# Kernel tuning notes

Hardware: AMD Instinct MI355X
Metric: run time of the kernel (lower is better)

The kernel has to match this reference:

```python
import jax, jax.numpy as jnp
import numpy as np
from jax import lax

B, C, H, W = 4, 128, 128, 128
DG = 2          # deformable groups
K = 9           # 3x3 kernel
EPS = 1e-5


def conv2d(x, w, stride=1, pad=1):
    return lax.conv_general_dilated(
        x, w, (stride, stride), [(pad, pad), (pad, pad)],
        dimension_numbers=("NCHW", "OIHW", "NCHW"))


def bn(x, p):
    # p: [4, C] = gamma, beta, running_mean, running_var (eval-mode BN)
    g, b, m, v = p[0], p[1], p[2], p[3]
    inv = g / jnp.sqrt(v + EPS)
    return x * inv[:, None, None] + (b - m * inv)[:, None, None]


def deform_sample(x, py, px):
    # x: [B,C,H,W]; py/px: [B,DG,K,H,W] absolute sample coords
    Bb, Cc, Hh, Ww = x.shape
    Cg = Cc // DG
    xg = x.reshape(Bb, DG, Cg, Hh * Ww)
    y0 = jnp.floor(py); x0 = jnp.floor(px)
    fy = py - y0; fx = px - x0
    y0i = y0.astype(jnp.int32); x0i = x0.astype(jnp.int32)

    def corner(yi, xi, wgt):
        valid = (yi >= 0) & (yi < Hh) & (xi >= 0) & (xi < Ww)
        idx = (jnp.clip(yi, 0, Hh - 1) * Ww + jnp.clip(xi, 0, Ww - 1)).reshape(Bb, DG, -1)
        v = jnp.take_along_axis(xg, idx[:, :, None, :], axis=3)  # [B,DG,Cg,K*H*W]
        return v * (wgt * valid).reshape(Bb, DG, 1, -1)

    val = (corner(y0i, x0i, (1 - fy) * (1 - fx))
           + corner(y0i, x0i + 1, (1 - fy) * fx)
           + corner(y0i + 1, x0i, fy * (1 - fx))
           + corner(y0i + 1, x0i + 1, fy * fx))
    return val.reshape(Bb, DG, Cg, K, Hh, Ww)


def modulated_deform_conv(x, off_w, off_b, dc_w, dc_b):
    Bb, Cc, Hh, Ww = x.shape
    off_out = conv2d(x, off_w) + off_b[None, :, None, None]   # [B,3*DG*K,H,W]
    o = off_out[:, :2 * DG * K].reshape(Bb, DG, K, 2, Hh, Ww)
    mask = jax.nn.sigmoid(off_out[:, 2 * DG * K:]).reshape(Bb, DG, K, Hh, Ww)
    ky = (jnp.arange(K) // 3 - 1).astype(x.dtype)
    kx = (jnp.arange(K) % 3 - 1).astype(x.dtype)
    iy = jnp.arange(Hh, dtype=x.dtype)[:, None]
    ix = jnp.arange(Ww, dtype=x.dtype)[None, :]
    py = o[:, :, :, 0] + iy + ky[None, None, :, None, None]
    px = o[:, :, :, 1] + ix + kx[None, None, :, None, None]
    g = deform_sample(x, py, px) * mask[:, :, None]            # [B,DG,Cg,K,H,W]
    wr = dc_w.reshape(dc_w.shape[0], DG, Cc // DG, K)          # [O,DG,Cg,K]
    out = jnp.einsum("odck,bdckhw->bohw", wr, g)
    return out + dc_b[None, :, None, None]


def setup_inputs() -> dict:
    key = jax.random.key(0)
    ks = jax.random.split(key, 16)
    s3 = 1.0 / np.sqrt(C * 9)
    s1 = 1.0 / np.sqrt(C)

    def bn_params(k):
        k1, k2, k3, k4 = jax.random.split(k, 4)
        return jnp.stack([
            jax.random.uniform(k1, (C,)) + 0.5,
            jax.random.normal(k2, (C,)) * 0.1,
            jax.random.normal(k3, (C,)) * 0.1,
            jax.random.uniform(k4, (C,)) + 0.5])

    return {
        "x": jax.random.normal(ks[0], (B, C, H, W), jnp.float32),
        "rb_w1": jax.random.normal(ks[1], (C, C, 3, 3), jnp.float32) * s3,
        "rb_b1": jax.random.normal(ks[2], (C,), jnp.float32) * 0.01,
        "rb_bn1": bn_params(ks[3]),
        "rb_w2": jax.random.normal(ks[4], (C, C, 3, 3), jnp.float32) * s3,
        "rb_b2": jax.random.normal(ks[5], (C,), jnp.float32) * 0.01,
        "rb_bn2": bn_params(ks[6]),
        "off_w": jax.random.normal(ks[7], (3 * DG * K, C, 3, 3), jnp.float32) * s3 * 0.1,
        "off_b": jax.random.normal(ks[8], (3 * DG * K,), jnp.float32) * 0.01,
        "dc_w": jax.random.normal(ks[9], (C, C, 3, 3), jnp.float32) * s3,
        "dc_b": jax.random.normal(ks[10], (C,), jnp.float32) * 0.01,
        "bn1": bn_params(ks[11]),
        "cv2_w": jax.random.normal(ks[12], (C, C, 1, 1), jnp.float32) * s1,
        "bn2": bn_params(ks[13]),
    }


def reference(x, rb_w1, rb_b1, rb_bn1, rb_w2, rb_b2, rb_bn2,
              off_w, off_b, dc_w, dc_b, bn1, cv2_w, bn2):
    # ResBlock (stride=1, n_in==n_out -> identity shortcut)
    h = jax.nn.relu(bn(conv2d(x, rb_w1) + rb_b1[None, :, None, None], rb_bn1))
    h = bn(conv2d(h, rb_w2) + rb_b2[None, :, None, None], rb_bn2)
    h = jax.nn.relu(h + x)
    # modulated deformable conv + BN + LeakyReLU(0.1)
    h = modulated_deform_conv(h, off_w, off_b, dc_w, dc_b)
    h = jax.nn.leaky_relu(bn(h, bn1), 0.1)
    # 1x1 conv (no bias) + BN + LeakyReLU(0.1)
    h = jax.nn.leaky_relu(bn(conv2d(h, cv2_w, pad=0), bn2), 0.1)
    # residual (downsample is None: in==out, stride==1)
    return x + h
```

## Files before the change

kernel.cpp:

```cpp
#include <hip/hip_runtime.h>
#include <math.h>

#define BB 4
#define EPSV 1e-5f

typedef __attribute__((ext_vector_type(8))) short short8;
typedef __attribute__((ext_vector_type(4))) float floatx4;
typedef __attribute__((ext_vector_type(4))) int intx4;
typedef __attribute__((ext_vector_type(4))) unsigned short ushort4v;

__device__ inline float b2f(unsigned short u) {
    unsigned v = ((unsigned)u) << 16;
    return __builtin_bit_cast(float, v);
}
__device__ inline unsigned short f2b(float f) {
    unsigned u = __builtin_bit_cast(unsigned, f);
    u += 0x7FFFu + ((u >> 16) & 1u);
    return (unsigned short)(u >> 16);
}
__device__ inline unsigned short f2b_fast(float f) {
    unsigned u = __builtin_bit_cast(unsigned, f);
    return (unsigned short)((u + 0x8000u) >> 16);
}

__global__ __launch_bounds__(256) void prep_k(
    const float* __restrict__ x, unsigned short* __restrict__ xb,
    const float* __restrict__ rb_w1, unsigned short* __restrict__ wf1,
    const float* __restrict__ rb_w2, unsigned short* __restrict__ wf2,
    const float* __restrict__ off_w, unsigned short* __restrict__ wfO,
    const float* __restrict__ dc_w, unsigned short* __restrict__ wfD,
    const float* __restrict__ cv2_w, unsigned short* __restrict__ wfC)
{
    __shared__ unsigned short t[64][136];
    const int bid = blockIdx.x;
    const int tid = threadIdx.x;

    if (bid < 1024) {
        const int px0 = (bid & 255) * 64;
        const int b = bid >> 8;
        const int pxr = tid & 63;
        const int c0 = tid >> 6;
#pragma unroll
        for (int i = 0; i < 32; ++i) {
            int c = c0 + i * 4;
            float v = x[(((size_t)b * 128 + c) << 14) + px0 + pxr];
            t[pxr][c] = f2b(v);
        }
        __syncthreads();
#pragma unroll
        for (int i = 0; i < 4; ++i) {
            int idx = tid + i * 256;
            int px = idx >> 4;
            int c8 = idx & 15;
            short8 v = *(const short8*)&t[px][c8 * 8];
            *(short8*)&xb[(((size_t)b << 14) + px0 + px) * 128 + c8 * 8] = v;
        }
        return;
    }
    if (bid < 2464) {
        const float* w; unsigned short* dst; int MPAD, OCH, t0;
        if (bid < 1600)      { w = rb_w1; dst = wf1; MPAD = 128; OCH = 128; t0 = 1024; }
        else if (bid < 2176) { w = rb_w2; dst = wf2; MPAD = 128; OCH = 128; t0 = 1600; }
        else                 { w = off_w; dst = wfO; MPAD = 64;  OCH = 54;  t0 = 2176; }
        int tt = (bid - t0) * 256 + tid;
        if (tt >= 1152 * MPAD) return;
        const int NMT2 = MPAD / 16;
        int j = tt & 7, lane = (tt >> 3) & 63, rest = tt >> 9;
        int mt = rest % NMT2, step = rest / NMT2;
        int oc = mt * 16 + (lane & 15);
        int k = step * 32 + ((lane >> 4) << 3) + j;
        int half = k / 576;
        int tap = (k - half * 576) >> 6;
        int c = half * 64 + (k & 63);
        float v = (oc < OCH) ? w[((size_t)oc * 128 + c) * 9 + tap] : 0.f;
        dst[tt] = f2b(v);
        return;
    }
    if (bid < 3040) {
        int tt = (bid - 2464) * 256 + tid;
        int j = tt & 7, lane = (tt >> 3) & 63, rest = tt >> 9;
        int mt = rest & 7, step = rest >> 3;
        int oc = mt * 16 + (lane & 15);
        int k = step * 32 + ((lane >> 4) << 3) + j;
        int dk = k >> 6, c = k & 63;
        int d = (dk >= 9) ? 1 : 0;
        int kk = dk - d * 9;
        wfD[tt] = f2b(dc_w[((size_t)oc * 128 + d * 64 + c) * 9 + kk]);
        return;
    }
    {
        int tt = (bid - 3040) * 256 + tid;
        int j = tt & 7, lane = (tt >> 3) & 63, rest = tt >> 9;
        int mt = rest & 7, step = rest >> 3;
        int oc = mt * 16 + (lane & 15);
        int k = step * 32 + ((lane >> 4) << 3) + j;
        wfC[tt] = f2b(cv2_w[oc * 128 + k]);
    }
}

template<int NMT, int MODE>
__global__ __launch_bounds__(256, 2) void conv3x3_mfma(
    const unsigned short* __restrict__ in, const unsigned short* __restrict__ wf,
    const float* __restrict__ bias, const float* __restrict__ bnp,
    const float* __restrict__ res, void* __restrict__ outv)
{
    __shared__ unsigned short sm[3][130][72];
    const int tid = threadIdx.x;
    const int lane = tid & 63, wid = tid >> 6;
    const int wm = wid & 1, wn = wid >> 1;
    const int h = blockIdx.x;
    const int b = blockIdx.y;
    const int n16 = lane & 15, quad = lane >> 4;

    short8 L[13];

    auto stage_load = [&](int half) {
#pragma unroll
        for (int rnd = 0; rnd < 13; ++rnd) {
            int idx = rnd * 256 + tid;
            short8 v = {0, 0, 0, 0, 0, 0, 0, 0};
            if (idx < 3120) {
                int c8 = idx & 7;
                int wl = (idx >> 3) % 130;
                int r  = (idx >> 3) / 130;
                int hh = h - 1 + r, ww = wl - 1;
                if ((unsigned)hh < 128u && (unsigned)ww < 128u)
                    v = *(const short8*)&in[(((size_t)b << 14) + hh * 128 + ww) * 128 + half * 64 + c8 * 8];
            }
            L[rnd] = v;
        }
    };
    auto stage_write = [&]() {
#pragma unroll
        for (int rnd = 0; rnd < 13; ++rnd) {
            int idx = rnd * 256 + tid;
            if (idx < 3120) {
                int c8 = idx & 7;
                int wl = (idx >> 3) % 130;
                int r  = (idx >> 3) / 130;
                *(short8*)&sm[r][wl][c8 * 8] = L[rnd];
            }
        }
    };

    floatx4 acc[NMT][4];
#pragma unroll
    for (int mt = 0; mt < NMT; ++mt)
#pragma unroll
        for (int nt = 0; nt < 4; ++nt)
            acc[mt][nt] = (floatx4){0.f, 0.f, 0.f, 0.f};

    auto compute = [&](int half) {
#pragma unroll
        for (int tap = 0; tap < 9; ++tap) {
            const int ky = tap / 3, kx = tap % 3;
#pragma unroll
            for (int cc = 0; cc < 2; ++cc) {
                const int step = half * 18 + tap * 2 + cc;
                short8 a[NMT], bf[4];
#pragma unroll
                for (int nt = 0; nt < 4; ++nt)
                    bf[nt] = *(const short8*)&sm[ky][wn * 64 + nt * 16 + n16 + kx][cc * 32 + quad * 8];
#pragma unroll
                for (int mt = 0; mt < NMT; ++mt)
                    a[mt] = *(const short8*)&wf[((size_t)(step * (2 * NMT) + wm * NMT + mt) * 64 + lane) * 8];
#pragma unroll
                for (int mt = 0; mt < NMT; ++mt)
#pragma unroll
                    for (int nt = 0; nt < 4; ++nt)
                        acc[mt][nt] = __builtin_amdgcn_mfma_f32_16x16x32_bf16(a[mt], bf[nt], acc[mt][nt], 0, 0, 0);
            }
        }
    };

    stage_load(0);
    stage_write();
    __syncthreads();
    stage_load(1);
    compute(0);
    __syncthreads();
    stage_write();
    __syncthreads();
    compute(1);

#pragma unroll
    for (int mt = 0; mt < NMT; ++mt) {
        const int ocb = (wm * NMT + mt) * 16 + quad * 4;
        float Ae[4], Be[4];
#pragma unroll
        for (int r = 0; r < 4; ++r) {
            int oc = ocb + r;
            if (MODE == 0) {
                Ae[r] = 1.f;
                Be[r] = (oc < 54) ? bias[oc] : 0.f;
            } else {
                float g = bnp[oc], be = bnp[128 + oc], m = bnp[256 + oc], vv = bnp[384 + oc];
                float inv = g * rsqrtf(vv + EPSV);
                Ae[r] = inv;
                Be[r] = be - m * inv + bias[oc] * inv;
            }
        }
#pragma unroll
        for (int nt = 0; nt < 4; ++nt) {
            int pxg = h * 128 + wn * 64 + nt * 16 + n16;
            if (MODE == 0) {
                float* outf = (float*)outv;
#pragma unroll
                for (int r = 0; r < 4; ++r) {
                    int oc = ocb + r;
                    if (oc < 54)
                        outf[(((size_t)(b * 54 + oc)) << 14) + pxg] = acc[mt][nt][r] + Be[r];
                }
            } else {
                ushort4v pk;
#pragma unroll
                for (int r = 0; r < 4; ++r) {
                    float v = acc[mt][nt][r] * Ae[r] + Be[r];
                    if (MODE == 2) v += res[(((size_t)b * 128 + ocb + r) << 14) + pxg];
                    v = fmaxf(v, 0.f);
                    pk[r] = f2b(v);
                }
                *(ushort4v*)&((unsigned short*)outv)[((size_t)((b << 14) + pxg)) * 128 + ocb] = pk;
            }
        }
    }
}

__global__ __launch_bounds__(256, 3) void deform_mfma(
    const unsigned short* __restrict__ src, const float* __restrict__ off,
    const unsigned short* __restrict__ wf, const float* __restrict__ dcb,
    const float* __restrict__ bnp, unsigned short* __restrict__ out)
{
    __shared__ unsigned short gt[2][64][72];
    __shared__ floatx4 smw[3][64];
    __shared__ intx4   sma[3][64];
    const int tid = threadIdx.x;
    const int lane = tid & 63, wid = tid >> 6;
    const int wm = wid & 1, wn = wid >> 1;
    const int w0 = (blockIdx.x & 1) * 64;
    const int h = blockIdx.x >> 1;
    const int b = blockIdx.y;
    const int n16 = lane & 15, quad = lane >> 4;
    const int q = tid & 7;
    const int pxq = (tid >> 3) & 31;

    const char* srcbyte = (const char*)src + ((size_t)b << 22);
    const float* offpx = off + (((size_t)(b * 54)) << 14) + h * 128 + w0 + tid;

    auto math = [&](int dk, int slot) {
        float oy = offpx[(size_t)(2 * dk) << 14];
        float ox = offpx[(size_t)(2 * dk + 1) << 14];
        float mz = offpx[(size_t)(36 + dk) << 14];
        int d = (dk >= 9) ? 1 : 0;
        int kk = dk - d * 9;
        float ms = 1.f / (1.f + __expf(-mz));
        float py = oy + (float)h + (float)(kk / 3 - 1);
        float pxs = ox + (float)(w0 + tid) + (float)(kk % 3 - 1);
        float y0f = floorf(py), x0f = floorf(pxs);
        float fy = py - y0f, fx = pxs - x0f;
        int y0 = (int)y0f, x0 = (int)x0f;
        int y1 = y0 + 1, x1 = x0 + 1;
        float w00 = (1.f - fy) * (1.f - fx) * ms, w01 = (1.f - fy) * fx * ms;
        float w10 = fy * (1.f - fx) * ms, w11 = fy * fx * ms;
        if ((unsigned)y0 >= 128u) { w00 = 0.f; w01 = 0.f; }
        if ((unsigned)y1 >= 128u) { w10 = 0.f; w11 = 0.f; }
        if ((unsigned)x0 >= 128u) { w00 = 0.f; w10 = 0.f; }
        if ((unsigned)x1 >= 128u) { w01 = 0.f; w11 = 0.f; }
        int y0c = min(max(y0, 0), 127), y1c = min(max(y1, 0), 127);
        int x0c = min(max(x0, 0), 127), x1c = min(max(x1, 0), 127);
        int chb = d * 128;
        smw[slot][tid] = (floatx4){w00, w01, w10, w11};
        sma[slot][tid] = (intx4){((y0c * 128 + x0c) << 8) + chb, ((y0c * 128 + x1c) << 8) + chb,
                                 ((y1c * 128 + x0c) << 8) + chb, ((y1c * 128 + x1c) << 8) + chb};
    };

    floatx4 wA[2];
    short8 g[2][4];
    auto gather = [&](int slot) {
#pragma unroll
        for (int ph = 0; ph < 2; ++ph) {
            int pxl = ph * 32 + pxq;
            floatx4 wv = smw[slot][pxl];
            intx4 av = sma[slot][pxl];
            wA[ph] = wv;
#pragma unroll
            for (int c = 0; c < 4; ++c)
                g[ph][c] = *(const short8*)(srcbyte + (size_t)(av[c] + q * 16));
        }
    };

    floatx4 acc[4][2];
#pragma unroll
    for (int mt = 0; mt < 4; ++mt)
#pragma unroll
        for (int nt = 0; nt < 2; ++nt)
            acc[mt][nt] = (floatx4){0.f, 0.f, 0.f, 0.f};

    if (tid < 64) { math(0, 0); math(1, 1); }
    __syncthreads();
    gather(0);

    int buf = 0;
    for (int dk = 0; dk < 18; ++dk) {
#pragma unroll
        for (int ph = 0; ph < 2; ++ph) {
            short8 o8;
#pragma unroll
            for (int j = 0; j < 8; ++j) {
                float v = wA[ph][0] * b2f((unsigned short)g[ph][0][j])
                        + wA[ph][1] * b2f((unsigned short)g[ph][1][j])
                        + wA[ph][2] * b2f((unsigned short)g[ph][2][j])
                        + wA[ph][3] * b2f((unsigned short)g[ph][3][j]);
                o8[j] = (short)f2b_fast(v);
            }
            *(short8*)&gt[buf][ph * 32 + pxq][q * 8] = o8;
        }
        if (tid < 64 && dk < 16) math(dk + 2, (dk + 2) % 3);
        __syncthreads();
        if (dk < 17) gather((dk + 1) % 3);

#pragma unroll
        for (int hf = 0; hf < 2; ++hf) {
            int s = dk * 2 + hf;
            short8 a[4], bfr[2];
#pragma unroll
            for (int nt = 0; nt < 2; ++nt)
                bfr[nt] = *(const short8*)&gt[buf][wn * 32 + nt * 16 + n16][hf * 32 + quad * 8];
#pragma unroll
            for (int mt = 0; mt < 4; ++mt)
                a[mt] = *(const short8*)&wf[((size_t)(s * 8 + wm * 4 + mt) * 64 + lane) * 8];
#pragma unroll
            for (int mt = 0; mt < 4; ++mt)
#pragma unroll
                for (int nt = 0; nt < 2; ++nt)
                    acc[mt][nt] = __builtin_amdgcn_mfma_f32_16x16x32_bf16(a[mt], bfr[nt], acc[mt][nt], 0, 0, 0);
        }
        buf ^= 1;
    }

#pragma unroll
    for (int mt = 0; mt < 4; ++mt) {
        const int ocb = (wm * 4 + mt) * 16 + quad * 4;
        float Ae[4], Be[4];
#pragma unroll
        for (int r = 0; r < 4; ++r) {
            int oc = ocb + r;
            float gg = bnp[oc], be = bnp[128 + oc], m = bnp[256 + oc], vv = bnp[384 + oc];
            float inv = gg * rsqrtf(vv + EPSV);
            Ae[r] = inv;
            Be[r] = be - m * inv + dcb[oc] * inv;
        }
#pragma unroll
        for (int nt = 0; nt < 2; ++nt) {
            int pxg2 = h * 128 + w0 + wn * 32 + nt * 16 + n16;
            ushort4v pk;
#pragma unroll
            for (int r = 0; r < 4; ++r) {
                float v = acc[mt][nt][r] * Ae[r] + Be[r];
                v = (v > 0.f) ? v : 0.1f * v;
                pk[r] = f2b(v);
            }
            *(ushort4v*)&out[((size_t)((b << 14) + pxg2)) * 128 + ocb] = pk;
        }
    }
}

__global__ __launch_bounds__(256, 4) void conv1x1_mfma(
    const unsigned short* __restrict__ in, const unsigned short* __restrict__ wf,
    const float* __restrict__ bnp, const float* __restrict__ x, float* __restrict__ out)
{
    const int tid = threadIdx.x;
    const int lane = tid & 63, wid = tid >> 6;
    const int wm = wid & 1, wn = wid >> 1;
    const int w0 = (blockIdx.x & 1) * 64;
    const int h = blockIdx.x >> 1;
    const int b = blockIdx.y;
    const int n16 = lane & 15, quad = lane >> 4;

    floatx4 acc[4][2];
#pragma unroll
    for (int mt = 0; mt < 4; ++mt)
#pragma unroll
        for (int nt = 0; nt < 2; ++nt)
            acc[mt][nt] = (floatx4){0.f, 0.f, 0.f, 0.f};

#pragma unroll
    for (int s = 0; s < 4; ++s) {
        short8 a[4], bfr[2];
#pragma unroll
        for (int nt = 0; nt < 2; ++nt) {
            int px = h * 128 + w0 + wn * 32 + nt * 16 + n16;
            bfr[nt] = *(const short8*)&in[((size_t)((b << 14) + px)) * 128 + s * 32 + quad * 8];
        }
#pragma unroll
        for (int mt = 0; mt < 4; ++mt)
            a[mt] = *(const short8*)&wf[((size_t)(s * 8 + wm * 4 + mt) * 64 + lane) * 8];
#pragma unroll
        for (int mt = 0; mt < 4; ++mt)
#pragma unroll
            for (int nt = 0; nt < 2; ++nt)
                acc[mt][nt] = __builtin_amdgcn_mfma_f32_16x16x32_bf16(a[mt], bfr[nt], acc[mt][nt], 0, 0, 0);
    }

#pragma unroll
    for (int mt = 0; mt < 4; ++mt) {
        const int ocb = (wm * 4 + mt) * 16 + quad * 4;
        float Ae[4], Be[4];
#pragma unroll
        for (int r = 0; r < 4; ++r) {
            int oc = ocb + r;
            float g = bnp[oc], be = bnp[128 + oc], m = bnp[256 + oc], vv = bnp[384 + oc];
            float inv = g * rsqrtf(vv + EPSV);
            Ae[r] = inv;
            Be[r] = be - m * inv;
        }
#pragma unroll
        for (int nt = 0; nt < 2; ++nt) {
            int pxg2 = h * 128 + w0 + wn * 32 + nt * 16 + n16;
#pragma unroll
            for (int r = 0; r < 4; ++r) {
                int oc = ocb + r;
                float v = acc[mt][nt][r] * Ae[r] + Be[r];
                v = (v > 0.f) ? v : 0.1f * v;
                v += x[(((size_t)b * 128 + oc) << 14) + pxg2];
                out[(((size_t)b * 128 + oc) << 14) + pxg2] = v;
            }
        }
    }
}

extern "C" void kernel_launch(void* const* d_in, const int* in_sizes, int n_in,
                              void* d_out, int out_size, void* d_ws, size_t ws_size,
                              hipStream_t stream) {
    const float* x      = (const float*)d_in[0];
    const float* rb_w1  = (const float*)d_in[1];
    const float* rb_b1  = (const float*)d_in[2];
    const float* rb_bn1 = (const float*)d_in[3];
    const float* rb_w2  = (const float*)d_in[4];
    const float* rb_b2  = (const float*)d_in[5];
    const float* rb_bn2 = (const float*)d_in[6];
    const float* off_w  = (const float*)d_in[7];
    const float* off_b  = (const float*)d_in[8];
    const float* dc_w   = (const float*)d_in[9];
    const float* dc_b   = (const float*)d_in[10];
    const float* bn1    = (const float*)d_in[11];
    const float* cv2_w  = (const float*)d_in[12];
    const float* bn2    = (const float*)d_in[13];

    char* base = (char*)d_ws;
    const size_t TSZ = (size_t)4 * 16384 * 128 * 2;
    unsigned short* xb = (unsigned short*)base;
    unsigned short* h1 = (unsigned short*)(base + TSZ);
    unsigned short* h2 = (unsigned short*)(base + 2 * TSZ);
    unsigned short* wf1 = (unsigned short*)(base + 3 * TSZ);
    unsigned short* wf2 = wf1 + 1152 * 128;
    unsigned short* wfO = wf2 + 1152 * 128;
    unsigned short* wfD = wfO + 1152 * 64;
    unsigned short* wfC = wfD + 1152 * 128;
    float* offb = (float*)h1;
    unsigned short* h3 = xb;

    dim3 blk(256, 1, 1);
    dim3 grid(256, BB, 1);
    dim3 grid3(128, BB, 1);

    prep_k<<<3104, 256, 0, stream>>>(x, xb, rb_w1, wf1, rb_w2, wf2,
                                     off_w, wfO, dc_w, wfD, cv2_w, wfC);

    conv3x3_mfma<4, 1><<<grid3, blk, 0, stream>>>(xb, wf1, rb_b1, rb_bn1, nullptr, (void*)h1);
    conv3x3_mfma<4, 2><<<grid3, blk, 0, stream>>>(h1, wf2, rb_b2, rb_bn2, x, (void*)h2);
    conv3x3_mfma<2, 0><<<grid3, blk, 0, stream>>>(h2, wfO, off_b, nullptr, nullptr, (void*)offb);
    deform_mfma<<<grid, blk, 0, stream>>>(h2, offb, wfD, dc_b, bn1, h3);
    conv1x1_mfma<<<grid, blk, 0, stream>>>(h3, wfC, bn2, x, (float*)d_out);
}
```

Measured before the change: 267.4 us.

## Fuse 1x1 conv into deform kernel, pipeline 3x3 conv over 32-channel phases

```diff
diff --git a/kernel.cpp b/kernel.cpp
--- a/kernel.cpp
+++ b/kernel.cpp
@@ -69,9 +69,8 @@
         int mt = rest % NMT2, step = rest / NMT2;
         int oc = mt * 16 + (lane & 15);
         int k = step * 32 + ((lane >> 4) << 3) + j;
-        int half = k / 576;
-        int tap = (k - half * 576) >> 6;
-        int c = half * 64 + (k & 63);
+        int phase = step / 9, tap = step % 9;
+        int c = phase * 32 + (k & 31);
         float v = (oc < OCH) ? w[((size_t)oc * 128 + c) * 9 + tap] : 0.f;
         dst[tt] = f2b(v);
         return;
@@ -99,12 +98,12 @@
 }
 
 template<int NMT, int MODE>
-__global__ __launch_bounds__(256, 2) void conv3x3_mfma(
+__global__ __launch_bounds__(256, 3) void conv3x3_mfma(
     const unsigned short* __restrict__ in, const unsigned short* __restrict__ wf,
     const float* __restrict__ bias, const float* __restrict__ bnp,
-    const float* __restrict__ res, void* __restrict__ outv)
+    const unsigned short* __restrict__ res, void* __restrict__ outv)
 {
-    __shared__ unsigned short sm[3][130][72];
+    __shared__ unsigned short sm[2][3][130][40];
     const int tid = threadIdx.x;
     const int lane = tid & 63, wid = tid >> 6;
     const int wm = wid & 1, wn = wid >> 1;
@@ -112,33 +111,32 @@
     const int b = blockIdx.y;
     const int n16 = lane & 15, quad = lane >> 4;
 
-    short8 L[13];
-
-    auto stage_load = [&](int half) {
-#pragma unroll
-        for (int rnd = 0; rnd < 13; ++rnd) {
+    short8 L[7];
+    auto stage_load = [&](int phase) {
+#pragma unroll
+        for (int rnd = 0; rnd < 7; ++rnd) {
             int idx = rnd * 256 + tid;
             short8 v = {0, 0, 0, 0, 0, 0, 0, 0};
-            if (idx < 3120) {
-                int c8 = idx & 7;
-                int wl = (idx >> 3) % 130;
-                int r  = (idx >> 3) / 130;
+            if (idx < 1560) {
+                int c8 = idx & 3;
+                int wl = (idx >> 2) % 130;
+                int r  = (idx >> 2) / 130;
                 int hh = h - 1 + r, ww = wl - 1;
                 if ((unsigned)hh < 128u && (unsigned)ww < 128u)
-                    v = *(const short8*)&in[(((size_t)b << 14) + hh * 128 + ww) * 128 + half * 64 + c8 * 8];
+                    v = *(const short8*)&in[(((size_t)b << 14) + hh * 128 + ww) * 128 + phase * 32 + c8 * 8];
             }
             L[rnd] = v;
         }
     };
-    auto stage_write = [&]() {
-#pragma unroll
-        for (int rnd = 0; rnd < 13; ++rnd) {
+    auto stage_write = [&](int buf) {
+#pragma unroll
+        for (int rnd = 0; rnd < 7; ++rnd) {
             int idx = rnd * 256 + tid;
-            if (idx < 3120) {
-                int c8 = idx & 7;
-                int wl = (idx >> 3) % 130;
-                int r  = (idx >> 3) / 130;
-                *(short8*)&sm[r][wl][c8 * 8] = L[rnd];
+            if (idx < 1560) {
+                int c8 = idx & 3;
+                int wl = (idx >> 2) % 130;
+                int r  = (idx >> 2) / 130;
+                *(short8*)&sm[buf][r][wl][c8 * 8] = L[rnd];
             }
         }
     };
@@ -150,38 +148,38 @@
         for (int nt = 0; nt < 4; ++nt)
             acc[mt][nt] = (floatx4){0.f, 0.f, 0.f, 0.f};
 
-    auto compute = [&](int half) {
+    auto compute = [&](int phase, int buf) {
 #pragma unroll
         for (int tap = 0; tap < 9; ++tap) {
             const int ky = tap / 3, kx = tap % 3;
-#pragma unroll
-            for (int cc = 0; cc < 2; ++cc) {
-                const int step = half * 18 + tap * 2 + cc;
-                short8 a[NMT], bf[4];
+            const int step = phase * 9 + tap;
+            short8 a[NMT], bf[4];
+#pragma unroll
+            for (int nt = 0; nt < 4; ++nt)
+                bf[nt] = *(const short8*)&sm[buf][ky][wn * 64 + nt * 16 + n16 + kx][quad * 8];
+#pragma unroll
+            for (int mt = 0; mt < NMT; ++mt)
+                a[mt] = *(const short8*)&wf[((size_t)(step * (2 * NMT) + wm * NMT + mt) * 64 + lane) * 8];
+#pragma unroll
+            for (int mt = 0; mt < NMT; ++mt)
 #pragma unroll
                 for (int nt = 0; nt < 4; ++nt)
-                    bf[nt] = *(const short8*)&sm[ky][wn * 64 + nt * 16 + n16 + kx][cc * 32 + quad * 8];
-#pragma unroll
-                for (int mt = 0; mt < NMT; ++mt)
-                    a[mt] = *(const short8*)&wf[((size_t)(step * (2 * NMT) + wm * NMT + mt) * 64 + lane) * 8];
-#pragma unroll
-                for (int mt = 0; mt < NMT; ++mt)
-#pragma unroll
-                    for (int nt = 0; nt < 4; ++nt)
-                        acc[mt][nt] = __builtin_amdgcn_mfma_f32_16x16x32_bf16(a[mt], bf[nt], acc[mt][nt], 0, 0, 0);
-            }
+                    acc[mt][nt] = __builtin_amdgcn_mfma_f32_16x16x32_bf16(a[mt], bf[nt], acc[mt][nt], 0, 0, 0);
         }
     };
 
     stage_load(0);
-    stage_write();
+    stage_write(0);
     __syncthreads();
-    stage_load(1);
-    compute(0);
-    __syncthreads();
-    stage_write();
-    __syncthreads();
-    compute(1);
+#pragma unroll
+    for (int p = 0; p < 4; ++p) {
+        if (p < 3) stage_load(p + 1);
+        compute(p, p & 1);
+        if (p < 3) {
+            stage_write((p + 1) & 1);
+            __syncthreads();
+        }
+    }
 
 #pragma unroll
     for (int mt = 0; mt < NMT; ++mt) {
@@ -212,11 +210,14 @@
                         outf[(((size_t)(b * 54 + oc)) << 14) + pxg] = acc[mt][nt][r] + Be[r];
                 }
             } else {
+                ushort4v rv = {0, 0, 0, 0};
+                if (MODE == 2)
+                    rv = *(const ushort4v*)&res[((size_t)((b << 14) + pxg)) * 128 + ocb];
                 ushort4v pk;
 #pragma unroll
                 for (int r = 0; r < 4; ++r) {
                     float v = acc[mt][nt][r] * Ae[r] + Be[r];
-                    if (MODE == 2) v += res[(((size_t)b * 128 + ocb + r) << 14) + pxg];
+                    if (MODE == 2) v += b2f(rv[r]);
                     v = fmaxf(v, 0.f);
                     pk[r] = f2b(v);
                 }
@@ -226,14 +227,17 @@
     }
 }
 
-__global__ __launch_bounds__(256, 3) void deform_mfma(
+__global__ __launch_bounds__(256, 3) void deform_fused(
     const unsigned short* __restrict__ src, const float* __restrict__ off,
     const unsigned short* __restrict__ wf, const float* __restrict__ dcb,
-    const float* __restrict__ bnp, unsigned short* __restrict__ out)
+    const float* __restrict__ bnp1, const unsigned short* __restrict__ wfC,
+    const float* __restrict__ bnp2, const unsigned short* __restrict__ xres,
+    float* __restrict__ out)
 {
     __shared__ unsigned short gt[2][64][72];
     __shared__ floatx4 smw[3][64];
     __shared__ intx4   sma[3][64];
+    __shared__ unsigned short ot[64][136];
     const int tid = threadIdx.x;
     const int lane = tid & 63, wid = tid >> 6;
     const int wm = wid & 1, wn = wid >> 1;
@@ -345,14 +349,14 @@
 #pragma unroll
         for (int r = 0; r < 4; ++r) {
             int oc = ocb + r;
-            float gg = bnp[oc], be = bnp[128 + oc], m = bnp[256 + oc], vv = bnp[384 + oc];
+            float gg = bnp1[oc], be = bnp1[128 + oc], m = bnp1[256 + oc], vv = bnp1[384 + oc];
             float inv = gg * rsqrtf(vv + EPSV);
             Ae[r] = inv;
             Be[r] = be - m * inv + dcb[oc] * inv;
         }
 #pragma unroll
         for (int nt = 0; nt < 2; ++nt) {
-            int pxg2 = h * 128 + w0 + wn * 32 + nt * 16 + n16;
+            int pxl = wn * 32 + nt * 16 + n16;
             ushort4v pk;
 #pragma unroll
             for (int r = 0; r < 4; ++r) {
@@ -360,46 +364,32 @@
                 v = (v > 0.f) ? v : 0.1f * v;
                 pk[r] = f2b(v);
             }
-            *(ushort4v*)&out[((size_t)((b << 14) + pxg2)) * 128 + ocb] = pk;
-        }
-    }
-}
-
-__global__ __launch_bounds__(256, 4) void conv1x1_mfma(
-    const unsigned short* __restrict__ in, const unsigned short* __restrict__ wf,
-    const float* __restrict__ bnp, const float* __restrict__ x, float* __restrict__ out)
-{
-    const int tid = threadIdx.x;
-    const int lane = tid & 63, wid = tid >> 6;
-    const int wm = wid & 1, wn = wid >> 1;
-    const int w0 = (blockIdx.x & 1) * 64;
-    const int h = blockIdx.x >> 1;
-    const int b = blockIdx.y;
-    const int n16 = lane & 15, quad = lane >> 4;
-
-    floatx4 acc[4][2];
+            *(ushort4v*)&ot[pxl][ocb] = pk;
+        }
+    }
+    __syncthreads();
+
+    floatx4 acc1[4][2];
 #pragma unroll
     for (int mt = 0; mt < 4; ++mt)
 #pragma unroll
         for (int nt = 0; nt < 2; ++nt)
-            acc[mt][nt] = (floatx4){0.f, 0.f, 0.f, 0.f};
+            acc1[mt][nt] = (floatx4){0.f, 0.f, 0.f, 0.f};
 
 #pragma unroll
     for (int s = 0; s < 4; ++s) {
         short8 a[4], bfr[2];
 #pragma unroll
-        for (int nt = 0; nt < 2; ++nt) {
-            int px = h * 128 + w0 + wn * 32 + nt * 16 + n16;
-            bfr[nt] = *(const short8*)&in[((size_t)((b << 14) + px)) * 128 + s * 32 + quad * 8];
-        }
+        for (int nt = 0; nt < 2; ++nt)
+            bfr[nt] = *(const short8*)&ot[wn * 32 + nt * 16 + n16][s * 32 + quad * 8];
 #pragma unroll
         for (int mt = 0; mt < 4; ++mt)
-            a[mt] = *(const short8*)&wf[((size_t)(s * 8 + wm * 4 + mt) * 64 + lane) * 8];
+            a[mt] = *(const short8*)&wfC[((size_t)(s * 8 + wm * 4 + mt) * 64 + lane) * 8];
 #pragma unroll
         for (int mt = 0; mt < 4; ++mt)
 #pragma unroll
             for (int nt = 0; nt < 2; ++nt)
-                acc[mt][nt] = __builtin_amdgcn_mfma_f32_16x16x32_bf16(a[mt], bfr[nt], acc[mt][nt], 0, 0, 0);
+                acc1[mt][nt] = __builtin_amdgcn_mfma_f32_16x16x32_bf16(a[mt], bfr[nt], acc1[mt][nt], 0, 0, 0);
     }
 
 #pragma unroll
@@ -409,20 +399,21 @@
 #pragma unroll
         for (int r = 0; r < 4; ++r) {
             int oc = ocb + r;
-            float g = bnp[oc], be = bnp[128 + oc], m = bnp[256 + oc], vv = bnp[384 + oc];
-            float inv = g * rsqrtf(vv + EPSV);
+            float gg = bnp2[oc], be = bnp2[128 + oc], m = bnp2[256 + oc], vv = bnp2[384 + oc];
+            float inv = gg * rsqrtf(vv + EPSV);
             Ae[r] = inv;
             Be[r] = be - m * inv;
         }
 #pragma unroll
         for (int nt = 0; nt < 2; ++nt) {
             int pxg2 = h * 128 + w0 + wn * 32 + nt * 16 + n16;
+            ushort4v rv = *(const ushort4v*)&xres[((size_t)((b << 14) + pxg2)) * 128 + ocb];
 #pragma unroll
             for (int r = 0; r < 4; ++r) {
                 int oc = ocb + r;
-                float v = acc[mt][nt][r] * Ae[r] + Be[r];
+                float v = acc1[mt][nt][r] * Ae[r] + Be[r];
                 v = (v > 0.f) ? v : 0.1f * v;
-                v += x[(((size_t)b * 128 + oc) << 14) + pxg2];
+                v += b2f(rv[r]);
                 out[(((size_t)b * 128 + oc) << 14) + pxg2] = v;
             }
         }
@@ -458,7 +449,6 @@
     unsigned short* wfD = wfO + 1152 * 64;
     unsigned short* wfC = wfD + 1152 * 128;
     float* offb = (float*)h1;
-    unsigned short* h3 = xb;
 
     dim3 blk(256, 1, 1);
     dim3 grid(256, BB, 1);
@@ -468,8 +458,7 @@
                                      off_w, wfO, dc_w, wfD, cv2_w, wfC);
 
     conv3x3_mfma<4, 1><<<grid3, blk, 0, stream>>>(xb, wf1, rb_b1, rb_bn1, nullptr, (void*)h1);
-    conv3x3_mfma<4, 2><<<grid3, blk, 0, stream>>>(h1, wf2, rb_b2, rb_bn2, x, (void*)h2);
+    conv3x3_mfma<4, 2><<<grid3, blk, 0, stream>>>(h1, wf2, rb_b2, rb_bn2, xb, (void*)h2);
     conv3x3_mfma<2, 0><<<grid3, blk, 0, stream>>>(h2, wfO, off_b, nullptr, nullptr, (void*)offb);
-    deform_mfma<<<grid, blk, 0, stream>>>(h2, offb, wfD, dc_b, bn1, h3);
-    conv1x1_mfma<<<grid, blk, 0, stream>>>(h3, wfC, bn2, x, (float*)d_out);
-}
+    deform_fused<<<grid, blk, 0, stream>>>(h2, offb, wfD, dc_b, bn1, wfC, bn2, xb, (float*)d_out);
+}
```

After: 274.3 us. 1.03x slower.

## Fuse the 1x1 conv into the deformable conv kernel and read bf16 residuals

Applied to the files above, without the earlier changes.

```diff
diff --git a/kernel.cpp b/kernel.cpp
--- a/kernel.cpp
+++ b/kernel.cpp
@@ -102,7 +102,7 @@
 __global__ __launch_bounds__(256, 2) void conv3x3_mfma(
     const unsigned short* __restrict__ in, const unsigned short* __restrict__ wf,
     const float* __restrict__ bias, const float* __restrict__ bnp,
-    const float* __restrict__ res, void* __restrict__ outv)
+    const unsigned short* __restrict__ res, void* __restrict__ outv)
 {
     __shared__ unsigned short sm[3][130][72];
     const int tid = threadIdx.x;
@@ -212,11 +212,14 @@
                         outf[(((size_t)(b * 54 + oc)) << 14) + pxg] = acc[mt][nt][r] + Be[r];
                 }
             } else {
+                ushort4v rv = {0, 0, 0, 0};
+                if (MODE == 2)
+                    rv = *(const ushort4v*)&res[((size_t)((b << 14) + pxg)) * 128 + ocb];
                 ushort4v pk;
 #pragma unroll
                 for (int r = 0; r < 4; ++r) {
                     float v = acc[mt][nt][r] * Ae[r] + Be[r];
-                    if (MODE == 2) v += res[(((size_t)b * 128 + ocb + r) << 14) + pxg];
+                    if (MODE == 2) v += b2f(rv[r]);
                     v = fmaxf(v, 0.f);
                     pk[r] = f2b(v);
                 }
@@ -226,14 +229,17 @@
     }
 }
 
-__global__ __launch_bounds__(256, 3) void deform_mfma(
+__global__ __launch_bounds__(256, 4) void deform_fused(
     const unsigned short* __restrict__ src, const float* __restrict__ off,
     const unsigned short* __restrict__ wf, const float* __restrict__ dcb,
-    const float* __restrict__ bnp, unsigned short* __restrict__ out)
+    const float* __restrict__ bnp1, const unsigned short* __restrict__ wfC,
+    const float* __restrict__ bnp2, const unsigned short* __restrict__ xres,
+    float* __restrict__ out)
 {
     __shared__ unsigned short gt[2][64][72];
     __shared__ floatx4 smw[3][64];
     __shared__ intx4   sma[3][64];
+    unsigned short (*ot)[136] = reinterpret_cast<unsigned short(*)[136]>(&gt[0][0][0]);
     const int tid = threadIdx.x;
     const int lane = tid & 63, wid = tid >> 6;
     const int wm = wid & 1, wn = wid >> 1;
@@ -338,6 +344,8 @@
         buf ^= 1;
     }
 
+    __syncthreads();
+
 #pragma unroll
     for (int mt = 0; mt < 4; ++mt) {
         const int ocb = (wm * 4 + mt) * 16 + quad * 4;
@@ -345,14 +353,14 @@
 #pragma unroll
         for (int r = 0; r < 4; ++r) {
             int oc = ocb + r;
-            float gg = bnp[oc], be = bnp[128 + oc], m = bnp[256 + oc], vv = bnp[384 + oc];
+            float gg = bnp1[oc], be = bnp1[128 + oc], m = bnp1[256 + oc], vv = bnp1[384 + oc];
             float inv = gg * rsqrtf(vv + EPSV);
             Ae[r] = inv;
             Be[r] = be - m * inv + dcb[oc] * inv;
         }
 #pragma unroll
         for (int nt = 0; nt < 2; ++nt) {
-            int pxg2 = h * 128 + w0 + wn * 32 + nt * 16 + n16;
+            int pxl = wn * 32 + nt * 16 + n16;
             ushort4v pk;
 #pragma unroll
             for (int r = 0; r < 4; ++r) {
@@ -360,46 +368,32 @@
                 v = (v > 0.f) ? v : 0.1f * v;
                 pk[r] = f2b(v);
             }
-            *(ushort4v*)&out[((size_t)((b << 14) + pxg2)) * 128 + ocb] = pk;
-        }
-    }
-}
-
-__global__ __launch_bounds__(256, 4) void conv1x1_mfma(
-    const unsigned short* __restrict__ in, const unsigned short* __restrict__ wf,
-    const float* __restrict__ bnp, const float* __restrict__ x, float* __restrict__ out)
-{
-    const int tid = threadIdx.x;
-    const int lane = tid & 63, wid = tid >> 6;
-    const int wm = wid & 1, wn = wid >> 1;
-    const int w0 = (blockIdx.x & 1) * 64;
-    const int h = blockIdx.x >> 1;
-    const int b = blockIdx.y;
-    const int n16 = lane & 15, quad = lane >> 4;
-
-    floatx4 acc[4][2];
+            *(ushort4v*)&ot[pxl][ocb] = pk;
+        }
+    }
+    __syncthreads();
+
+    floatx4 acc1[4][2];
 #pragma unroll
     for (int mt = 0; mt < 4; ++mt)
 #pragma unroll
         for (int nt = 0; nt < 2; ++nt)
-            acc[mt][nt] = (floatx4){0.f, 0.f, 0.f, 0.f};
+            acc1[mt][nt] = (floatx4){0.f, 0.f, 0.f, 0.f};
 
 #pragma unroll
     for (int s = 0; s < 4; ++s) {
         short8 a[4], bfr[2];
 #pragma unroll
-        for (int nt = 0; nt < 2; ++nt) {
-            int px = h * 128 + w0 + wn * 32 + nt * 16 + n16;
-            bfr[nt] = *(const short8*)&in[((size_t)((b << 14) + px)) * 128 + s * 32 + quad * 8];
-        }
+        for (int nt = 0; nt < 2; ++nt)
+            bfr[nt] = *(const short8*)&ot[wn * 32 + nt * 16 + n16][s * 32 + quad * 8];
 #pragma unroll
         for (int mt = 0; mt < 4; ++mt)
-            a[mt] = *(const short8*)&wf[((size_t)(s * 8 + wm * 4 + mt) * 64 + lane) * 8];
+            a[mt] = *(const short8*)&wfC[((size_t)(s * 8 + wm * 4 + mt) * 64 + lane) * 8];
 #pragma unroll
         for (int mt = 0; mt < 4; ++mt)
 #pragma unroll
             for (int nt = 0; nt < 2; ++nt)
-                acc[mt][nt] = __builtin_amdgcn_mfma_f32_16x16x32_bf16(a[mt], bfr[nt], acc[mt][nt], 0, 0, 0);
+                acc1[mt][nt] = __builtin_amdgcn_mfma_f32_16x16x32_bf16(a[mt], bfr[nt], acc1[mt][nt], 0, 0, 0);
     }
 
 #pragma unroll
@@ -409,20 +403,21 @@
 #pragma unroll
         for (int r = 0; r < 4; ++r) {
             int oc = ocb + r;
-            float g = bnp[oc], be = bnp[128 + oc], m = bnp[256 + oc], vv = bnp[384 + oc];
-            float inv = g * rsqrtf(vv + EPSV);
+            float gg = bnp2[oc], be = bnp2[128 + oc], m = bnp2[256 + oc], vv = bnp2[384 + oc];
+            float inv = gg * rsqrtf(vv + EPSV);
             Ae[r] = inv;
             Be[r] = be - m * inv;
         }
 #pragma unroll
         for (int nt = 0; nt < 2; ++nt) {
             int pxg2 = h * 128 + w0 + wn * 32 + nt * 16 + n16;
+            ushort4v rv = *(const ushort4v*)&xres[((size_t)((b << 14) + pxg2)) * 128 + ocb];
 #pragma unroll
             for (int r = 0; r < 4; ++r) {
                 int oc = ocb + r;
-                float v = acc[mt][nt][r] * Ae[r] + Be[r];
+                float v = acc1[mt][nt][r] * Ae[r] + Be[r];
                 v = (v > 0.f) ? v : 0.1f * v;
-                v += x[(((size_t)b * 128 + oc) << 14) + pxg2];
+                v += b2f(rv[r]);
                 out[(((size_t)b * 128 + oc) << 14) + pxg2] = v;
             }
         }
@@ -458,7 +453,6 @@
     unsigned short* wfD = wfO + 1152 * 64;
     unsigned short* wfC = wfD + 1152 * 128;
     float* offb = (float*)h1;
-    unsigned short* h3 = xb;
 
     dim3 blk(256, 1, 1);
     dim3 grid(256, BB, 1);
@@ -468,8 +462,7 @@
                                      off_w, wfO, dc_w, wfD, cv2_w, wfC);
 
     conv3x3_mfma<4, 1><<<grid3, blk, 0, stream>>>(xb, wf1, rb_b1, rb_bn1, nullptr, (void*)h1);
-    conv3x3_mfma<4, 2><<<grid3, blk, 0, stream>>>(h1, wf2, rb_b2, rb_bn2, x, (void*)h2);
+    conv3x3_mfma<4, 2><<<grid3, blk, 0, stream>>>(h1, wf2, rb_b2, rb_bn2, xb, (void*)h2);
     conv3x3_mfma<2, 0><<<grid3, blk, 0, stream>>>(h2, wfO, off_b, nullptr, nullptr, (void*)offb);
-    deform_mfma<<<grid, blk, 0, stream>>>(h2, offb, wfD, dc_b, bn1, h3);
-    conv1x1_mfma<<<grid, blk, 0, stream>>>(h3, wfC, bn2, x, (float*)d_out);
-}
+    deform_fused<<<grid, blk, 0, stream>>>(h2, offb, wfD, dc_b, bn1, wfC, bn2, xb, (float*)d_out);
+}
```

Result: faster. 248.6 us (-7.0%).
